# Optimization experiments

Hardware: AMD Instinct MI355X
Metric: run time of the kernel (lower is better)

The kernel has to match this reference:

```python
import jax, jax.numpy as jnp
import numpy as np

N_NODES = 50000
EPS = 1e-7      # GENConv message epsilon
BN_EPS = 1e-5   # BatchNorm1d eps
N_AGGR = 2


def setup_inputs() -> dict:
    key = jax.random.key(0)
    ks = jax.random.split(key, 8)
    C = 64
    E = 800000
    x = jax.random.normal(ks[0], (N_NODES, C), dtype=jnp.float32)
    edge_index = jax.random.randint(ks[1], (2, E), 0, N_NODES, dtype=jnp.int64)
    # per-GENConv MLP params, stacked over the N_AGGR layers
    W1 = jax.random.normal(ks[2], (N_AGGR, C, 2 * C), dtype=jnp.float32) * (1.0 / np.sqrt(C))
    b1 = jnp.zeros((N_AGGR, 2 * C), dtype=jnp.float32)
    gamma = jnp.ones((N_AGGR, 2 * C), dtype=jnp.float32)
    beta = jnp.zeros((N_AGGR, 2 * C), dtype=jnp.float32)
    W2 = jax.random.normal(ks[3], (N_AGGR, 2 * C, C), dtype=jnp.float32) * (1.0 / np.sqrt(2 * C))
    b2 = jnp.zeros((N_AGGR, C), dtype=jnp.float32)
    t = jnp.ones((N_AGGR,), dtype=jnp.float32)  # learnable softmax temperature
    return {"x": x, "edge_index": edge_index, "W1": W1, "b1": b1,
            "gamma": gamma, "beta": beta, "W2": W2, "b2": b2, "t": t}


def _gen_conv(x, src, dst, W1_l, b1_l, gamma_l, beta_l, W2_l, b2_l, t_l):
    # message: relu(x_j) + eps  (edge_attr is None)
    m = jax.nn.relu(x[src]) + EPS                      # [E, C]
    # softmax aggregation over edges grouped by destination node
    logits = m * t_l                                   # [E, C]
    seg_max = jax.ops.segment_max(logits, dst, num_segments=N_NODES)  # [N, C]
    ex = jnp.exp(logits - seg_max[dst])                # [E, C]
    den = jax.ops.segment_sum(ex, dst, num_segments=N_NODES)          # [N, C]
    alpha = ex / (den[dst] + 1e-16)                    # [E, C]
    aggr = jax.ops.segment_sum(m * alpha, dst, num_segments=N_NODES)  # [N, C]
    # residual then MLP: Linear(C,2C) -> BatchNorm1d (train-mode stats) -> ReLU -> Linear(2C,C)
    h = aggr + x
    h = h @ W1_l + b1_l                                # [N, 2C]
    mean = h.mean(axis=0)
    var = h.var(axis=0)                                # biased variance (torch BN)
    h = (h - mean) / jnp.sqrt(var + BN_EPS) * gamma_l + beta_l
    h = jax.nn.relu(h)
    h = h @ W2_l + b2_l                                # [N, C]
    return h


def reference(x, edge_index, W1, b1, gamma, beta, W2, b2, t):
    src = edge_index[0]
    dst = edge_index[1]
    for l in range(N_AGGR):
        x = _gen_conv(x, src, dst, W1[l], b1[l], gamma[l], beta[l], W2[l], b2[l], t[l])
        x = jax.nn.relu(x)
        # dropout in eval mode == identity
    return x
```

## Files before the change

kernel.cpp:

```cpp
#include <hip/hip_runtime.h>
#include <math.h>

#define NN 50000
#define EPSM 1e-7f
#define BN_EPS 1e-5f
#define NBK 391
#define LOG2E 1.44269504088896340736f

#define BN_REP 32
#define MM_REP 8


__global__ __launch_bounds__(256) void bucket_hist_kernel(
    const int* __restrict__ dst, int* __restrict__ bhist, int E,
    unsigned* __restrict__ mm0, float* __restrict__ bn0){
  __shared__ int h[NBK];
  int t = threadIdx.x;
  if (blockIdx.x == 0){
    for (int i = t; i < MM_REP * 128; i += 256)
      mm0[i] = ((i & 127) < 64) ? 0x7F7FFFFFu : 0u;
    for (int i = t; i < BN_REP * 256; i += 256) bn0[i] = 0.f;
  }
  for (int i = t; i < NBK; i += 256) h[i] = 0;
  __syncthreads();
  int e0 = blockIdx.x * 4096;
  int cnt = min(4096, E - e0);
  for (int i = t; i < cnt; i += 256) atomicAdd(&h[dst[e0 + i] >> 7], 1);
  __syncthreads();
  for (int i = t; i < NBK; i += 256) if (h[i]) atomicAdd(&bhist[i], h[i]);
}

__global__ void bucket_scan_kernel(const int* __restrict__ bhist,
                                   int* __restrict__ bbase, int* __restrict__ gcur){
  int lane = threadIdx.x;
  int loc[7]; int s = 0;
#pragma unroll
  for (int k = 0; k < 7; ++k){
    int i = lane * 7 + k;
    int v = (i < NBK) ? bhist[i] : 0;
    loc[k] = s; s += v;
  }
  int sc = s;
#pragma unroll
  for (int o = 1; o < 64; o <<= 1){
    int n = __shfl_up(sc, o);
    if (lane >= o) sc += n;
  }
  int exc = sc - s;
#pragma unroll
  for (int k = 0; k < 7; ++k){
    int i = lane * 7 + k;
    if (i < NBK){ bbase[i] = exc + loc[k]; gcur[i] = exc + loc[k]; }
    else if (i == NBK) bbase[i] = exc + loc[k];
  }
}

__global__ __launch_bounds__(256) void bucket_scatter_kernel(
    const int* __restrict__ src, const int* __restrict__ dst,
    int* __restrict__ gcur, unsigned* __restrict__ packed_g, int E){
  __shared__ int hist[NBK], offs[NBK], gb[NBK], curk[NBK];
  __shared__ unsigned stage[4096];
  __shared__ int gpos[4096];
  int t = threadIdx.x;
  for (int i = t; i < NBK; i += 256) hist[i] = 0;
  __syncthreads();
  int e0 = blockIdx.x * 4096;
  int cnt = min(4096, E - e0);
  unsigned pk[16]; int bk[16];
  int nmine = 0;
  for (int i = t; i < cnt; i += 256){
    int d = dst[e0 + i], s = src[e0 + i];
    pk[nmine] = ((unsigned)d << 16) | (unsigned)s;
    bk[nmine] = d >> 7;
    atomicAdd(&hist[bk[nmine]], 1);
    ++nmine;
  }
  __syncthreads();
  if (t < 64){
    int loc[7]; int s = 0;
#pragma unroll
    for (int k = 0; k < 7; ++k){
      int i = t * 7 + k;
      int v = (i < NBK) ? hist[i] : 0;
      loc[k] = s; s += v;
    }
    int sc = s;
#pragma unroll
    for (int o = 1; o < 64; o <<= 1){
      int n = __shfl_up(sc, o);
      if (t >= o) sc += n;
    }
    int exc = sc - s;
#pragma unroll
    for (int k = 0; k < 7; ++k){
      int i = t * 7 + k;
      if (i < NBK) offs[i] = exc + loc[k];
    }
  }
  __syncthreads();
  for (int i = t; i < NBK; i += 256){
    int h = hist[i];
    gb[i] = h ? atomicAdd(&gcur[i], h) : 0;
    curk[i] = offs[i];
  }
  __syncthreads();
  for (int k = 0; k < nmine; ++k){
    int b = bk[k];
    int p = atomicAdd(&curk[b], 1);
    stage[p] = pk[k];
    gpos[p] = gb[b] + (p - offs[b]);
  }
  __syncthreads();
  for (int j = t; j < cnt; j += 256) packed_g[gpos[j]] = stage[j];
}

__global__ __launch_bounds__(256) void bucket_place_kernel(
    const unsigned* __restrict__ packed_g, const int* __restrict__ bbase,
    int* __restrict__ start_g, int* __restrict__ end_g,
    unsigned short* __restrict__ srcs_g, int N){
  __shared__ int deg[128], off[128], cur[128];
  __shared__ int sstage[4096];
  int b = blockIdx.x, t = threadIdx.x;
  int beg = bbase[b], cnt = bbase[b + 1] - beg;
  if (t < 128) deg[t] = 0;
  __syncthreads();
  for (int j = t; j < cnt; j += 256)
    atomicAdd(&deg[(packed_g[beg + j] >> 16) & 127], 1);
  __syncthreads();
  if (t < 64){
    int i0 = t * 2;
    int v0 = deg[i0], v1 = deg[i0 + 1];
    int s = v0 + v1;
    int sc = s;
#pragma unroll
    for (int o = 1; o < 64; o <<= 1){
      int n = __shfl_up(sc, o);
      if (t >= o) sc += n;
    }
    int exc = sc - s;
    off[i0] = exc; off[i0 + 1] = exc + v0;
  }
  __syncthreads();
  int node0 = b * 128;
  if (t < 128){
    int node = node0 + t;
    if (node < N){
      start_g[node] = beg + off[t];
      end_g[node] = beg + off[t] + deg[t];
    }
    cur[t] = off[t];
  }
  __syncthreads();
  if (cnt <= 4096){
    for (int j = t; j < cnt; j += 256){
      unsigned p = packed_g[beg + j];
      int lp = atomicAdd(&cur[(p >> 16) & 127], 1);
      sstage[lp] = (int)(p & 0xFFFFu);
    }
    __syncthreads();
    for (int j = t; j < cnt; j += 256)
      srcs_g[beg + j] = (unsigned short)sstage[j];
  } else {
    for (int j = t; j < cnt; j += 256){
      unsigned p = packed_g[beg + j];
      int lp = atomicAdd(&cur[(p >> 16) & 127], 1);
      srcs_g[beg + lp] = (unsigned short)(p & 0xFFFFu);
    }
  }
}


__global__ __launch_bounds__(256) void colminmax_kernel(
    const float* __restrict__ x, unsigned* __restrict__ mm,
    unsigned short* __restrict__ mh, int N){
  __shared__ unsigned smn[256], smx[256];
  int c = threadIdx.x & 63;
  int slot = blockIdx.x * 4 + (threadIdx.x >> 6);
  float mx = 0.f, mn = 1e30f;
  for (int r = slot; r < N; r += 256 * 4){
    float m = fmaxf(x[r * 64 + c], 0.f) + EPSM;
    unsigned u = __float_as_uint(m);
    u += 0x7FFFu + ((u >> 16) & 1u);
    unsigned short us = (unsigned short)(u >> 16);
    mh[r * 64 + c] = us;
    float mb = __uint_as_float(((unsigned)us) << 16);
    mx = fmaxf(mx, mb);
    mn = fminf(mn, mb);
  }
  smn[threadIdx.x] = __float_as_uint(mn);
  smx[threadIdx.x] = __float_as_uint(mx);
  __syncthreads();
  if (threadIdx.x < 64){
    int rep = (blockIdx.x & (MM_REP - 1)) * 128;
    unsigned a = smn[c], b = smn[c + 64], d = smn[c + 128], e = smn[c + 192];
    atomicMin(&mm[rep + c], min(min(a, b), min(d, e)));
    a = smx[c]; b = smx[c + 64]; d = smx[c + 128]; e = smx[c + 192];
    atomicMax(&mm[rep + 64 + c], max(max(a, b), max(d, e)));
  }
}


__global__ __launch_bounds__(256) void aggregate_kernel(
    const float* __restrict__ x, const unsigned* __restrict__ mh32,
    const int* __restrict__ start, const int* __restrict__ segend,
    const unsigned short* __restrict__ srcs, const float* __restrict__ tptr,
    int layer, const unsigned* __restrict__ mm, float* __restrict__ h0, int N){
  int node = blockIdx.x * 4 + (threadIdx.x >> 6);
  if (node >= N) return;
  int lane = threadIdx.x & 63;
  int half = lane >> 5, cp = lane & 31;
  float t2 = tptr[layer] * LOG2E;
  unsigned uMnL = 0x7F7FFFFFu, uMxL = 0u, uMnH = 0x7F7FFFFFu, uMxH = 0u;
#pragma unroll
  for (int r = 0; r < MM_REP; ++r){
    const unsigned* mr = mm + r * 128;
    uMnL = min(uMnL, mr[2 * cp]);       uMxL = max(uMxL, mr[64 + 2 * cp]);
    uMnH = min(uMnH, mr[2 * cp + 1]);   uMxH = max(uMxH, mr[64 + 2 * cp + 1]);
  }
  float mnL = __uint_as_float(uMnL), mxL = __uint_as_float(uMxL);
  float mnH = __uint_as_float(uMnH), mxH = __uint_as_float(uMxH);
  float BL = fmaxf(t2 * mxL, t2 * mnL);
  float BH = fmaxf(t2 * mxH, t2 * mnH);
  int beg = start[node], end = segend[node];
  float dL0=0.f,dL1=0.f,dL2=0.f,dL3=0.f, nL0=0.f,nL1=0.f,nL2=0.f,nL3=0.f;
  float dH0=0.f,dH1=0.f,dH2=0.f,dH3=0.f, nH0=0.f,nH1=0.f,nH2=0.f,nH3=0.f;
  int e = beg + half;
  for (; e + 6 < end; e += 8){
    int s0 = srcs[e], s1 = srcs[e + 2], s2 = srcs[e + 4], s3 = srcs[e + 6];
    unsigned u0 = mh32[s0 * 32 + cp], u1 = mh32[s1 * 32 + cp];
    unsigned u2 = mh32[s2 * 32 + cp], u3 = mh32[s3 * 32 + cp];
    float mL0 = __uint_as_float(u0 << 16), mH0 = __uint_as_float(u0 & 0xFFFF0000u);
    float mL1 = __uint_as_float(u1 << 16), mH1 = __uint_as_float(u1 & 0xFFFF0000u);
    float mL2 = __uint_as_float(u2 << 16), mH2 = __uint_as_float(u2 & 0xFFFF0000u);
    float mL3 = __uint_as_float(u3 << 16), mH3 = __uint_as_float(u3 & 0xFFFF0000u);
    float pL0 = exp2f(mL0 * t2 - BL), pH0 = exp2f(mH0 * t2 - BH);
    float pL1 = exp2f(mL1 * t2 - BL), pH1 = exp2f(mH1 * t2 - BH);
    float pL2 = exp2f(mL2 * t2 - BL), pH2 = exp2f(mH2 * t2 - BH);
    float pL3 = exp2f(mL3 * t2 - BL), pH3 = exp2f(mH3 * t2 - BH);
    dL0 += pL0; nL0 += mL0 * pL0;  dH0 += pH0; nH0 += mH0 * pH0;
    dL1 += pL1; nL1 += mL1 * pL1;  dH1 += pH1; nH1 += mH1 * pH1;
    dL2 += pL2; nL2 += mL2 * pL2;  dH2 += pH2; nH2 += mH2 * pH2;
    dL3 += pL3; nL3 += mL3 * pL3;  dH3 += pH3; nH3 += mH3 * pH3;
  }
  for (; e < end; e += 2){
    int s = srcs[e];
    unsigned u = mh32[s * 32 + cp];
    float mL = __uint_as_float(u << 16), mH = __uint_as_float(u & 0xFFFF0000u);
    float pL = exp2f(mL * t2 - BL), pH = exp2f(mH * t2 - BH);
    dL0 += pL; nL0 += mL * pL;  dH0 += pH; nH0 += mH * pH;
  }
  float dL = (dL0 + dL1) + (dL2 + dL3), nL = (nL0 + nL1) + (nL2 + nL3);
  float dH = (dH0 + dH1) + (dH2 + dH3), nH = (nH0 + nH1) + (nH2 + nH3);
  dL += __shfl_xor(dL, 32); nL += __shfl_xor(nL, 32);
  dH += __shfl_xor(dH, 32); nH += __shfl_xor(nH, 32);
  if (half == 0){
    float2 xv = ((const float2*)x)[node * 32 + cp];
    float2 o;
    o.x = nL / (dL + 1e-16f) + xv.x;
    o.y = nH / (dH + 1e-16f) + xv.y;
    ((float2*)h0)[node * 32 + cp] = o;
  }
}


__global__ __launch_bounds__(256) void gemm1_kernel(
    const float* __restrict__ h0, const float* __restrict__ W1,
    const float* __restrict__ b1, float* __restrict__ h1,
    float* __restrict__ bn, int N,
    unsigned* __restrict__ mm_next, float* __restrict__ bn_next){
  __shared__ float a_lds[64 * 68];
  __shared__ float w_lds[64 * 128];
  int t = threadIdx.x;
  if (mm_next != 0 && blockIdx.x == 0){
    for (int i = t; i < MM_REP * 128; i += 256)
      mm_next[i] = ((i & 127) < 64) ? 0x7F7FFFFFu : 0u;
    for (int i = t; i < BN_REP * 256; i += 256) bn_next[i] = 0.f;
  }
  const float4* wg = (const float4*)W1;
  float4* wl = (float4*)w_lds;
#pragma unroll
  for (int i = 0; i < 8; ++i) wl[t + 256 * i] = wg[t + 256 * i];
  int row0 = blockIdx.x * 64;
#pragma unroll
  for (int i = 0; i < 4; ++i){
    int li = t + 256 * i;
    int r = li >> 4, q = li & 15;
    int gr = row0 + r;
    float4 v = make_float4(0.f, 0.f, 0.f, 0.f);
    if (gr < N) v = ((const float4*)h0)[gr * 16 + q];
    *(float4*)&a_lds[r * 68 + q * 4] = v;
  }
  __syncthreads();
  int tc = t & 31, tr = t >> 5;
  float4 bias = ((const float4*)b1)[tc];
  float acc[8][4];
#pragma unroll
  for (int r = 0; r < 8; ++r){
    acc[r][0] = bias.x; acc[r][1] = bias.y; acc[r][2] = bias.z; acc[r][3] = bias.w;
  }
  for (int k = 0; k < 64; k += 4){
    float4 w0 = *(const float4*)&w_lds[(k + 0) * 128 + tc * 4];
    float4 w1 = *(const float4*)&w_lds[(k + 1) * 128 + tc * 4];
    float4 w2 = *(const float4*)&w_lds[(k + 2) * 128 + tc * 4];
    float4 w3 = *(const float4*)&w_lds[(k + 3) * 128 + tc * 4];
#pragma unroll
    for (int r = 0; r < 8; ++r){
      float4 a = *(const float4*)&a_lds[(tr * 8 + r) * 68 + k];
      acc[r][0] += a.x * w0.x + a.y * w1.x + a.z * w2.x + a.w * w3.x;
      acc[r][1] += a.x * w0.y + a.y * w1.y + a.z * w2.y + a.w * w3.y;
      acc[r][2] += a.x * w0.z + a.y * w1.z + a.z * w2.z + a.w * w3.z;
      acc[r][3] += a.x * w0.w + a.y * w1.w + a.z * w2.w + a.w * w3.w;
    }
  }
  float s[4] = {0.f, 0.f, 0.f, 0.f}, s2[4] = {0.f, 0.f, 0.f, 0.f};
#pragma unroll
  for (int r = 0; r < 8; ++r){
    int gr = row0 + tr * 8 + r;
    if (gr < N){
      *(float4*)&h1[gr * 128 + tc * 4] =
          make_float4(acc[r][0], acc[r][1], acc[r][2], acc[r][3]);
#pragma unroll
      for (int j = 0; j < 4; ++j){ s[j] += acc[r][j]; s2[j] += acc[r][j] * acc[r][j]; }
    }
  }
  __syncthreads();
  float* red = a_lds;
  if (t < 256){ red[t] = 0.f; }
  __syncthreads();
#pragma unroll
  for (int j = 0; j < 4; ++j){
    atomicAdd(&red[tc * 4 + j], s[j]);
    atomicAdd(&red[128 + tc * 4 + j], s2[j]);
  }
  __syncthreads();
  if (t < 256) atomicAdd(&bn[(blockIdx.x & (BN_REP - 1)) * 256 + t], red[t]);
}

__global__ __launch_bounds__(256) void gemm2_kernel(
    const float* __restrict__ h1, const float* __restrict__ bn,
    const float* __restrict__ gamma, const float* __restrict__ beta, int layer,
    const float* __restrict__ W2, const float* __restrict__ b2,
    float* __restrict__ xout, int N,
    unsigned* __restrict__ mm_next, unsigned short* __restrict__ mh_next){
  __shared__ float a_lds[64 * 132];
  __shared__ float w_lds[128 * 68];
  __shared__ float ss[256];
  __shared__ unsigned smn[64], smx[64];
  int t = threadIdx.x;
  if (t < 128){
    float s = 0.f, s2 = 0.f;
#pragma unroll
    for (int r = 0; r < BN_REP; ++r){
      s  += bn[r * 256 + t];
      s2 += bn[r * 256 + 128 + t];
    }
    float mean = s * (1.f / (float)N);
    float var = s2 * (1.f / (float)N) - mean * mean;
    var = fmaxf(var, 0.f);
    float sc = gamma[layer * 128 + t] / sqrtf(var + BN_EPS);
    ss[t] = sc;
    ss[128 + t] = beta[layer * 128 + t] - mean * sc;
  }
  if (t < 64){ smn[t] = 0x7F7FFFFFu; smx[t] = 0u; }
  const float4* wg = (const float4*)W2;
#pragma unroll
  for (int i = 0; i < 8; ++i){
    int li = t + 256 * i;
    int k = li >> 4, q = li & 15;
    *(float4*)&w_lds[k * 68 + q * 4] = wg[li];
  }
  __syncthreads();
  int row0 = blockIdx.x * 64;
#pragma unroll
  for (int i = 0; i < 8; ++i){
    int li = t + 256 * i;
    int r = li >> 5, q = li & 31;
    int gr = row0 + r;
    float4 v = make_float4(0.f, 0.f, 0.f, 0.f);
    if (gr < N) v = ((const float4*)h1)[gr * 32 + q];
    float4 sc = *(const float4*)&ss[q * 4];
    float4 sh = *(const float4*)&ss[128 + q * 4];
    v.x = fmaxf(v.x * sc.x + sh.x, 0.f);
    v.y = fmaxf(v.y * sc.y + sh.y, 0.f);
    v.z = fmaxf(v.z * sc.z + sh.z, 0.f);
    v.w = fmaxf(v.w * sc.w + sh.w, 0.f);
    *(float4*)&a_lds[r * 132 + q * 4] = v;
  }
  __syncthreads();
  int tc = t & 15, tr = t >> 4;
  float4 bias = ((const float4*)b2)[tc];
  float acc[4][4];
#pragma unroll
  for (int r = 0; r < 4; ++r){
    acc[r][0] = bias.x; acc[r][1] = bias.y; acc[r][2] = bias.z; acc[r][3] = bias.w;
  }
  for (int k = 0; k < 128; k += 4){
    float4 w0 = *(const float4*)&w_lds[(k + 0) * 68 + tc * 4];
    float4 w1 = *(const float4*)&w_lds[(k + 1) * 68 + tc * 4];
    float4 w2 = *(const float4*)&w_lds[(k + 2) * 68 + tc * 4];
    float4 w3 = *(const float4*)&w_lds[(k + 3) * 68 + tc * 4];
#pragma unroll
    for (int r = 0; r < 4; ++r){
      float4 a = *(const float4*)&a_lds[(tr * 4 + r) * 132 + k];
      acc[r][0] += a.x * w0.x + a.y * w1.x + a.z * w2.x + a.w * w3.x;
      acc[r][1] += a.x * w0.y + a.y * w1.y + a.z * w2.y + a.w * w3.y;
      acc[r][2] += a.x * w0.z + a.y * w1.z + a.z * w2.z + a.w * w3.z;
      acc[r][3] += a.x * w0.w + a.y * w1.w + a.z * w2.w + a.w * w3.w;
    }
  }
  unsigned mnv[4] = {0x7F7FFFFFu, 0x7F7FFFFFu, 0x7F7FFFFFu, 0x7F7FFFFFu};
  unsigned mxv[4] = {0u, 0u, 0u, 0u};
#pragma unroll
  for (int r = 0; r < 4; ++r){
    int gr = row0 + tr * 4 + r;
    if (gr < N){
      float o0 = fmaxf(acc[r][0], 0.f), o1 = fmaxf(acc[r][1], 0.f);
      float o2 = fmaxf(acc[r][2], 0.f), o3 = fmaxf(acc[r][3], 0.f);
      *(float4*)&xout[gr * 64 + tc * 4] = make_float4(o0, o1, o2, o3);
      if (mh_next != 0){
        unsigned us[4];
        float ov[4] = {o0, o1, o2, o3};
#pragma unroll
        for (int j = 0; j < 4; ++j){
          unsigned u = __float_as_uint(ov[j] + EPSM);
          u += 0x7FFFu + ((u >> 16) & 1u);
          us[j] = u >> 16;
          unsigned fb = us[j] << 16;
          mnv[j] = min(mnv[j], fb);
          mxv[j] = max(mxv[j], fb);
        }
        ((uint2*)mh_next)[gr * 16 + tc] =
            make_uint2(us[0] | (us[1] << 16), us[2] | (us[3] << 16));
      }
    }
  }
  if (mh_next != 0){
    __syncthreads();
#pragma unroll
    for (int j = 0; j < 4; ++j){
      atomicMin(&smn[tc * 4 + j], mnv[j]);
      atomicMax(&smx[tc * 4 + j], mxv[j]);
    }
    __syncthreads();
    if (t < 64){
      int rep = (blockIdx.x & (MM_REP - 1)) * 128;
      atomicMin(&mm_next[rep + t], smn[t]);
      atomicMax(&mm_next[rep + 64 + t], smx[t]);
    }
  }
}

extern "C" void kernel_launch(void* const* d_in, const int* in_sizes, int n_in,
                              void* d_out, int out_size, void* d_ws, size_t ws_size,
                              hipStream_t stream) {
  const float* x0    = (const float*)d_in[0];
  const int*   ei    = (const int*)d_in[1];
  const float* W1    = (const float*)d_in[2];
  const float* b1    = (const float*)d_in[3];
  const float* gamma = (const float*)d_in[4];
  const float* beta  = (const float*)d_in[5];
  const float* W2    = (const float*)d_in[6];
  const float* b2    = (const float*)d_in[7];
  const float* tptr  = (const float*)d_in[8];

  const int N = NN;
  const int E = in_sizes[1] / 2;
  const int* src = ei;
  const int* dst = ei + E;

  float* ws  = (float*)d_ws;
  float* h0  = ws;
  float* h1  = h0 + N * 64;
  float* bn0 = h1 + N * 128;
  float* bn1 = bn0 + BN_REP * 256;
  unsigned* mm0 = (unsigned*)(bn1 + BN_REP * 256);
  unsigned* mm1 = mm0 + MM_REP * 128;
  unsigned short* mh = (unsigned short*)(mm1 + MM_REP * 128);
  int* bhist = (int*)(mh + N * 64);
  int* bbase = bhist + NBK;
  int* gcur  = bbase + NBK + 1;
  int* start = gcur + NBK;
  int* segend = start + N;
  unsigned* packed = (unsigned*)(segend + N);
  unsigned short* srcs = (unsigned short*)(packed + E);

  float* out = (float*)d_out;

  const int row_blocks = (N + 63) / 64;
  const int chunk_blocks = (E + 4095) / 4096;
  const int agg_blocks = (N + 3) / 4;

  hipMemsetAsync(bhist, 0, NBK * sizeof(int), stream);
  bucket_hist_kernel<<<chunk_blocks, 256, 0, stream>>>(dst, bhist, E, mm0, bn0);
  bucket_scan_kernel<<<1, 64, 0, stream>>>(bhist, bbase, gcur);
  bucket_scatter_kernel<<<chunk_blocks, 256, 0, stream>>>(src, dst, gcur, packed, E);
  bucket_place_kernel<<<NBK, 256, 0, stream>>>(packed, bbase, start, segend, srcs, N);

  colminmax_kernel<<<256, 256, 0, stream>>>(x0, mm0, mh, N);
  aggregate_kernel<<<agg_blocks, 256, 0, stream>>>(x0, (const unsigned*)mh, start,
                                                   segend, srcs, tptr, 0, mm0, h0, N);
  gemm1_kernel<<<row_blocks, 256, 0, stream>>>(h0, W1, b1, h1, bn0, N, mm1, bn1);
  gemm2_kernel<<<row_blocks, 256, 0, stream>>>(h1, bn0, gamma, beta, 0, W2, b2,
                                               out, N, mm1, mh);
  aggregate_kernel<<<agg_blocks, 256, 0, stream>>>(out, (const unsigned*)mh, start,
                                                   segend, srcs, tptr, 1, mm1, h0, N);
  gemm1_kernel<<<row_blocks, 256, 0, stream>>>(h0, W1 + 8192, b1 + 128, h1, bn1, N,
                                               (unsigned*)0, (float*)0);
  gemm2_kernel<<<row_blocks, 256, 0, stream>>>(h1, bn1, gamma, beta, 1, W2 + 8192,
                                               b2 + 64, out, N,
                                               (unsigned*)0, (unsigned short*)0);
}
```

Before: 326.5 us.

## Widen aggregate gathers to 8-byte loads and read GEMM weights from global

The aggregate kernel now gives each 64-lane wavefront four edge slots of 16 lanes. Each lane gathers a uint2 (four bf16 channels) per edge instead of a 32-bit word, which means fewer, wider gather transactions and a two-stage shuffle reduction. Separately, both GEMM kernels stop staging the weight matrix in LDS and read it straight from global/L2 as float4 inside the k loop. This removes the per-block weight copy and cuts LDS footprint, which may raise occupancy, but it relies on caches to serve the repeated weight reads.

```diff
diff --git a/kernel.cpp b/kernel.cpp
--- a/kernel.cpp
+++ b/kernel.cpp
@@ -201,64 +201,79 @@
 
 
 __global__ __launch_bounds__(256) void aggregate_kernel(
-    const float* __restrict__ x, const unsigned* __restrict__ mh32,
+    const float* __restrict__ x, const uint2* __restrict__ mh2,
     const int* __restrict__ start, const int* __restrict__ segend,
     const unsigned short* __restrict__ srcs, const float* __restrict__ tptr,
     int layer, const unsigned* __restrict__ mm, float* __restrict__ h0, int N){
   int node = blockIdx.x * 4 + (threadIdx.x >> 6);
   if (node >= N) return;
   int lane = threadIdx.x & 63;
-  int half = lane >> 5, cp = lane & 31;
+  int slot = lane >> 4, cp = lane & 15;
   float t2 = tptr[layer] * LOG2E;
-  unsigned uMnL = 0x7F7FFFFFu, uMxL = 0u, uMnH = 0x7F7FFFFFu, uMxH = 0u;
+  const uint4* mmv = (const uint4*)mm;
+  uint4 mn = make_uint4(0x7F7FFFFFu, 0x7F7FFFFFu, 0x7F7FFFFFu, 0x7F7FFFFFu);
+  uint4 mx = make_uint4(0u, 0u, 0u, 0u);
 #pragma unroll
   for (int r = 0; r < MM_REP; ++r){
-    const unsigned* mr = mm + r * 128;
-    uMnL = min(uMnL, mr[2 * cp]);       uMxL = max(uMxL, mr[64 + 2 * cp]);
-    uMnH = min(uMnH, mr[2 * cp + 1]);   uMxH = max(uMxH, mr[64 + 2 * cp + 1]);
-  }
-  float mnL = __uint_as_float(uMnL), mxL = __uint_as_float(uMxL);
-  float mnH = __uint_as_float(uMnH), mxH = __uint_as_float(uMxH);
-  float BL = fmaxf(t2 * mxL, t2 * mnL);
-  float BH = fmaxf(t2 * mxH, t2 * mnH);
+    uint4 a = mmv[r * 32 + cp];
+    uint4 b = mmv[r * 32 + 16 + cp];
+    mn.x = min(mn.x, a.x); mn.y = min(mn.y, a.y);
+    mn.z = min(mn.z, a.z); mn.w = min(mn.w, a.w);
+    mx.x = max(mx.x, b.x); mx.y = max(mx.y, b.y);
+    mx.z = max(mx.z, b.z); mx.w = max(mx.w, b.w);
+  }
+  float B0 = fmaxf(t2 * __uint_as_float(mx.x), t2 * __uint_as_float(mn.x));
+  float B1 = fmaxf(t2 * __uint_as_float(mx.y), t2 * __uint_as_float(mn.y));
+  float B2 = fmaxf(t2 * __uint_as_float(mx.z), t2 * __uint_as_float(mn.z));
+  float B3 = fmaxf(t2 * __uint_as_float(mx.w), t2 * __uint_as_float(mn.w));
   int beg = start[node], end = segend[node];
-  float dL0=0.f,dL1=0.f,dL2=0.f,dL3=0.f, nL0=0.f,nL1=0.f,nL2=0.f,nL3=0.f;
-  float dH0=0.f,dH1=0.f,dH2=0.f,dH3=0.f, nH0=0.f,nH1=0.f,nH2=0.f,nH3=0.f;
-  int e = beg + half;
-  for (; e + 6 < end; e += 8){
-    int s0 = srcs[e], s1 = srcs[e + 2], s2 = srcs[e + 4], s3 = srcs[e + 6];
-    unsigned u0 = mh32[s0 * 32 + cp], u1 = mh32[s1 * 32 + cp];
-    unsigned u2 = mh32[s2 * 32 + cp], u3 = mh32[s3 * 32 + cp];
-    float mL0 = __uint_as_float(u0 << 16), mH0 = __uint_as_float(u0 & 0xFFFF0000u);
-    float mL1 = __uint_as_float(u1 << 16), mH1 = __uint_as_float(u1 & 0xFFFF0000u);
-    float mL2 = __uint_as_float(u2 << 16), mH2 = __uint_as_float(u2 & 0xFFFF0000u);
-    float mL3 = __uint_as_float(u3 << 16), mH3 = __uint_as_float(u3 & 0xFFFF0000u);
-    float pL0 = exp2f(mL0 * t2 - BL), pH0 = exp2f(mH0 * t2 - BH);
-    float pL1 = exp2f(mL1 * t2 - BL), pH1 = exp2f(mH1 * t2 - BH);
-    float pL2 = exp2f(mL2 * t2 - BL), pH2 = exp2f(mH2 * t2 - BH);
-    float pL3 = exp2f(mL3 * t2 - BL), pH3 = exp2f(mH3 * t2 - BH);
-    dL0 += pL0; nL0 += mL0 * pL0;  dH0 += pH0; nH0 += mH0 * pH0;
-    dL1 += pL1; nL1 += mL1 * pL1;  dH1 += pH1; nH1 += mH1 * pH1;
-    dL2 += pL2; nL2 += mL2 * pL2;  dH2 += pH2; nH2 += mH2 * pH2;
-    dL3 += pL3; nL3 += mL3 * pL3;  dH3 += pH3; nH3 += mH3 * pH3;
-  }
-  for (; e < end; e += 2){
-    int s = srcs[e];
-    unsigned u = mh32[s * 32 + cp];
-    float mL = __uint_as_float(u << 16), mH = __uint_as_float(u & 0xFFFF0000u);
-    float pL = exp2f(mL * t2 - BL), pH = exp2f(mH * t2 - BH);
-    dL0 += pL; nL0 += mL * pL;  dH0 += pH; nH0 += mH * pH;
-  }
-  float dL = (dL0 + dL1) + (dL2 + dL3), nL = (nL0 + nL1) + (nL2 + nL3);
-  float dH = (dH0 + dH1) + (dH2 + dH3), nH = (nH0 + nH1) + (nH2 + nH3);
-  dL += __shfl_xor(dL, 32); nL += __shfl_xor(nL, 32);
-  dH += __shfl_xor(dH, 32); nH += __shfl_xor(nH, 32);
-  if (half == 0){
-    float2 xv = ((const float2*)x)[node * 32 + cp];
-    float2 o;
-    o.x = nL / (dL + 1e-16f) + xv.x;
-    o.y = nH / (dH + 1e-16f) + xv.y;
-    ((float2*)h0)[node * 32 + cp] = o;
+  float d0 = 0.f, d1 = 0.f, d2 = 0.f, d3 = 0.f;
+  float n0 = 0.f, n1 = 0.f, n2 = 0.f, n3 = 0.f;
+  int e = beg;
+  for (; e + 7 < end; e += 8){
+    int sA = srcs[e + slot];
+    int sB = srcs[e + 4 + slot];
+    uint2 uA = mh2[sA * 16 + cp];
+    uint2 uB = mh2[sB * 16 + cp];
+    float a0 = __uint_as_float(uA.x << 16), a1 = __uint_as_float(uA.x & 0xFFFF0000u);
+    float a2 = __uint_as_float(uA.y << 16), a3 = __uint_as_float(uA.y & 0xFFFF0000u);
+    float b0 = __uint_as_float(uB.x << 16), b1 = __uint_as_float(uB.x & 0xFFFF0000u);
+    float b2 = __uint_as_float(uB.y << 16), b3 = __uint_as_float(uB.y & 0xFFFF0000u);
+    float pA0 = exp2f(a0 * t2 - B0), pA1 = exp2f(a1 * t2 - B1);
+    float pA2 = exp2f(a2 * t2 - B2), pA3 = exp2f(a3 * t2 - B3);
+    float pB0 = exp2f(b0 * t2 - B0), pB1 = exp2f(b1 * t2 - B1);
+    float pB2 = exp2f(b2 * t2 - B2), pB3 = exp2f(b3 * t2 - B3);
+    d0 += pA0 + pB0; n0 += a0 * pA0 + b0 * pB0;
+    d1 += pA1 + pB1; n1 += a1 * pA1 + b1 * pB1;
+    d2 += pA2 + pB2; n2 += a2 * pA2 + b2 * pB2;
+    d3 += pA3 + pB3; n3 += a3 * pA3 + b3 * pB3;
+  }
+  for (; e + slot < end; e += 4){
+    int s = srcs[e + slot];
+    uint2 u = mh2[s * 16 + cp];
+    float a0 = __uint_as_float(u.x << 16), a1 = __uint_as_float(u.x & 0xFFFF0000u);
+    float a2 = __uint_as_float(u.y << 16), a3 = __uint_as_float(u.y & 0xFFFF0000u);
+    float p0 = exp2f(a0 * t2 - B0), p1 = exp2f(a1 * t2 - B1);
+    float p2 = exp2f(a2 * t2 - B2), p3 = exp2f(a3 * t2 - B3);
+    d0 += p0; n0 += a0 * p0;  d1 += p1; n1 += a1 * p1;
+    d2 += p2; n2 += a2 * p2;  d3 += p3; n3 += a3 * p3;
+  }
+  d0 += __shfl_xor(d0, 16); d1 += __shfl_xor(d1, 16);
+  d2 += __shfl_xor(d2, 16); d3 += __shfl_xor(d3, 16);
+  n0 += __shfl_xor(n0, 16); n1 += __shfl_xor(n1, 16);
+  n2 += __shfl_xor(n2, 16); n3 += __shfl_xor(n3, 16);
+  d0 += __shfl_xor(d0, 32); d1 += __shfl_xor(d1, 32);
+  d2 += __shfl_xor(d2, 32); d3 += __shfl_xor(d3, 32);
+  n0 += __shfl_xor(n0, 32); n1 += __shfl_xor(n1, 32);
+  n2 += __shfl_xor(n2, 32); n3 += __shfl_xor(n3, 32);
+  if (slot == 0){
+    float4 xv = ((const float4*)x)[node * 16 + cp];
+    float4 o;
+    o.x = n0 / (d0 + 1e-16f) + xv.x;
+    o.y = n1 / (d1 + 1e-16f) + xv.y;
+    o.z = n2 / (d2 + 1e-16f) + xv.z;
+    o.w = n3 / (d3 + 1e-16f) + xv.w;
+    ((float4*)h0)[node * 16 + cp] = o;
   }
 }
 
@@ -269,17 +284,12 @@
     float* __restrict__ bn, int N,
     unsigned* __restrict__ mm_next, float* __restrict__ bn_next){
   __shared__ float a_lds[64 * 68];
-  __shared__ float w_lds[64 * 128];
   int t = threadIdx.x;
   if (mm_next != 0 && blockIdx.x == 0){
     for (int i = t; i < MM_REP * 128; i += 256)
       mm_next[i] = ((i & 127) < 64) ? 0x7F7FFFFFu : 0u;
     for (int i = t; i < BN_REP * 256; i += 256) bn_next[i] = 0.f;
   }
-  const float4* wg = (const float4*)W1;
-  float4* wl = (float4*)w_lds;
-#pragma unroll
-  for (int i = 0; i < 8; ++i) wl[t + 256 * i] = wg[t + 256 * i];
   int row0 = blockIdx.x * 64;
 #pragma unroll
   for (int i = 0; i < 4; ++i){
@@ -298,11 +308,13 @@
   for (int r = 0; r < 8; ++r){
     acc[r][0] = bias.x; acc[r][1] = bias.y; acc[r][2] = bias.z; acc[r][3] = bias.w;
   }
+  const float4* wg = (const float4*)W1;
+#pragma unroll 2
   for (int k = 0; k < 64; k += 4){
-    float4 w0 = *(const float4*)&w_lds[(k + 0) * 128 + tc * 4];
-    float4 w1 = *(const float4*)&w_lds[(k + 1) * 128 + tc * 4];
-    float4 w2 = *(const float4*)&w_lds[(k + 2) * 128 + tc * 4];
-    float4 w3 = *(const float4*)&w_lds[(k + 3) * 128 + tc * 4];
+    float4 w0 = wg[(k + 0) * 32 + tc];
+    float4 w1 = wg[(k + 1) * 32 + tc];
+    float4 w2 = wg[(k + 2) * 32 + tc];
+    float4 w3 = wg[(k + 3) * 32 + tc];
 #pragma unroll
     for (int r = 0; r < 8; ++r){
       float4 a = *(const float4*)&a_lds[(tr * 8 + r) * 68 + k];
@@ -343,7 +355,6 @@
     float* __restrict__ xout, int N,
     unsigned* __restrict__ mm_next, unsigned short* __restrict__ mh_next){
   __shared__ float a_lds[64 * 132];
-  __shared__ float w_lds[128 * 68];
   __shared__ float ss[256];
   __shared__ unsigned smn[64], smx[64];
   int t = threadIdx.x;
@@ -362,13 +373,6 @@
     ss[128 + t] = beta[layer * 128 + t] - mean * sc;
   }
   if (t < 64){ smn[t] = 0x7F7FFFFFu; smx[t] = 0u; }
-  const float4* wg = (const float4*)W2;
-#pragma unroll
-  for (int i = 0; i < 8; ++i){
-    int li = t + 256 * i;
-    int k = li >> 4, q = li & 15;
-    *(float4*)&w_lds[k * 68 + q * 4] = wg[li];
-  }
   __syncthreads();
   int row0 = blockIdx.x * 64;
 #pragma unroll
@@ -394,11 +398,13 @@
   for (int r = 0; r < 4; ++r){
     acc[r][0] = bias.x; acc[r][1] = bias.y; acc[r][2] = bias.z; acc[r][3] = bias.w;
   }
+  const float4* wg = (const float4*)W2;
+#pragma unroll 2
   for (int k = 0; k < 128; k += 4){
-    float4 w0 = *(const float4*)&w_lds[(k + 0) * 68 + tc * 4];
-    float4 w1 = *(const float4*)&w_lds[(k + 1) * 68 + tc * 4];
-    float4 w2 = *(const float4*)&w_lds[(k + 2) * 68 + tc * 4];
-    float4 w3 = *(const float4*)&w_lds[(k + 3) * 68 + tc * 4];
+    float4 w0 = wg[(k + 0) * 16 + tc];
+    float4 w1 = wg[(k + 1) * 16 + tc];
+    float4 w2 = wg[(k + 2) * 16 + tc];
+    float4 w3 = wg[(k + 3) * 16 + tc];
 #pragma unroll
     for (int r = 0; r < 4; ++r){
       float4 a = *(const float4*)&a_lds[(tr * 4 + r) * 132 + k];
@@ -497,12 +503,12 @@
   bucket_place_kernel<<<NBK, 256, 0, stream>>>(packed, bbase, start, segend, srcs, N);
 
   colminmax_kernel<<<256, 256, 0, stream>>>(x0, mm0, mh, N);
-  aggregate_kernel<<<agg_blocks, 256, 0, stream>>>(x0, (const unsigned*)mh, start,
+  aggregate_kernel<<<agg_blocks, 256, 0, stream>>>(x0, (const uint2*)mh, start,
                                                    segend, srcs, tptr, 0, mm0, h0, N);
   gemm1_kernel<<<row_blocks, 256, 0, stream>>>(h0, W1, b1, h1, bn0, N, mm1, bn1);
   gemm2_kernel<<<row_blocks, 256, 0, stream>>>(h1, bn0, gamma, beta, 0, W2, b2,
                                                out, N, mm1, mh);
-  aggregate_kernel<<<agg_blocks, 256, 0, stream>>>(out, (const unsigned*)mh, start,
+  aggregate_kernel<<<agg_blocks, 256, 0, stream>>>(out, (const uint2*)mh, start,
                                                    segend, srcs, tptr, 1, mm1, h0, N);
   gemm1_kernel<<<row_blocks, 256, 0, stream>>>(h0, W1 + 8192, b1 + 128, h1, bn1, N,
                                                (unsigned*)0, (float*)0);
```

New measurement: 324.2 us. About the same (-0.7%).
